# Optimization experiments

Hardware: AMD Instinct MI355X
Metric: run time of the kernel (lower is better)

The kernel has to match this reference:

```python
import jax, jax.numpy as jnp
import numpy as np

B, S, D, H = 2, 2048, 1024, 16
DK = D // H  # 64
THETA = 10000.0
SCALE = 1.0 / np.sqrt(DK)


def _rope(t, pos):
    """Apply rotary embedding. t: [b,h,s,dk], pos: [b,s] int."""
    inv_freq = THETA ** (-jnp.arange(0, DK, 2, dtype=jnp.float32) / DK)  # [dk/2]
    ang = pos[:, None, :, None].astype(jnp.float32) * inv_freq  # [b,1,s,dk/2]
    cos, sin = jnp.cos(ang), jnp.sin(ang)
    t1, t2 = t[..., 0::2], t[..., 1::2]  # interleaved pairs
    rot = jnp.stack([t1 * cos - t2 * sin, t1 * sin + t2 * cos], axis=-1)
    return rot.reshape(t.shape)


def setup_inputs() -> dict:
    key = jax.random.key(0)
    ks = jax.random.split(key, 9)
    sc = 0.02
    x = jax.random.normal(ks[0], (B, S, D), jnp.float32)
    token_position = jnp.tile(jnp.arange(S, dtype=jnp.int32)[None, :], (B, 1))
    Wq = jax.random.normal(ks[1], (D, D), jnp.float32) * sc
    Wk = jax.random.normal(ks[2], (D, D), jnp.float32) * sc
    Wv = jax.random.normal(ks[3], (D, D), jnp.float32) * sc
    Wo = jax.random.normal(ks[4], (D, D), jnp.float32) * sc
    bq = jnp.zeros((D,), jnp.float32)
    bk = jnp.zeros((D,), jnp.float32)
    bv = jnp.zeros((D,), jnp.float32)
    bo = jnp.zeros((D,), jnp.float32)
    return {"x": x, "token_position": token_position,
            "Wq": Wq, "bq": bq, "Wk": Wk, "bk": bk,
            "Wv": Wv, "bv": bv, "Wo": Wo, "bo": bo}


def reference(x, token_position, Wq, bq, Wk, bk, Wv, bv, Wo, bo):
    b, s, d = x.shape
    # projections, split heads: [b,s,d] -> [b,h,s,dk]
    def heads(t):
        return t.reshape(b, s, H, DK).transpose(0, 2, 1, 3)
    q = heads(x @ Wq + bq)
    k = heads(x @ Wk + bk)
    v = heads(x @ Wv + bv)
    q = _rope(q, token_position)
    k = _rope(k, token_position)
    scores = jnp.einsum('bhnk,bhmk->bhnm', q, k) * SCALE  # [b,h,s,s]
    causal = jnp.tril(jnp.ones((s, s), dtype=bool))
    scores = jnp.where(causal, scores, -jnp.inf)
    probs = jax.nn.softmax(scores, axis=-1)
    o = jnp.einsum('bhnm,bhmk->bhnk', probs, v)  # [b,h,s,dk]
    o = o.transpose(0, 2, 1, 3).reshape(b, s, d)
    return o @ Wo + bo
```

## Files before the change

### kernel.cpp

```cpp
#include <hip/hip_runtime.h>
#include <math.h>

#define BB  2
#define SS  2048
#define DD  1024
#define HH  16
#define DKK 64

constexpr float kScale = 0.125f;
constexpr float kC1 = 0.18033688011112042f;
constexpr float kC2 = 23.0831206542234144f;

typedef __bf16 bf16x8 __attribute__((ext_vector_type(8)));
typedef __bf16 bf16x4 __attribute__((ext_vector_type(4)));
typedef float f32x4 __attribute__((ext_vector_type(4)));

__device__ __forceinline__ void async_copy16(const void* g, void* l) {
  __builtin_amdgcn_global_load_lds(
      (const __attribute__((address_space(1))) void*)g,
      (__attribute__((address_space(3))) void*)l, 16, 0, 0);
}

__global__ __launch_bounds__(256) void prep_kernel(
    const float* __restrict__ x, const int* __restrict__ pos,
    const float* __restrict__ W0, const float* __restrict__ W1,
    const float* __restrict__ W2, const float* __restrict__ W3,
    __bf16* __restrict__ xb, float2* __restrict__ rtab,
    __bf16* __restrict__ T0, __bf16* __restrict__ T1,
    __bf16* __restrict__ T2, __bf16* __restrict__ T3) {
  __shared__ __bf16 tile[64][65];
  const int bid = blockIdx.x;
  const int t = threadIdx.x;
  if (bid < 2048) {
    const size_t i = ((size_t)bid * 256 + t) * 8;
    const float4 v0 = *(const float4*)(x + i);
    const float4 v1 = *(const float4*)(x + i + 4);
    bf16x8 o;
    o[0] = (__bf16)v0.x; o[1] = (__bf16)v0.y; o[2] = (__bf16)v0.z; o[3] = (__bf16)v0.w;
    o[4] = (__bf16)v1.x; o[5] = (__bf16)v1.y; o[6] = (__bf16)v1.z; o[7] = (__bf16)v1.w;
    *(bf16x8*)(xb + i) = o;
  } else if (bid < 2560) {
    const int idx = (bid - 2048) * 256 + t;
    const int m = idx >> 5, pi = idx & 31;
    const float inv = exp2f(-0.4152410118609203f * (float)pi);
    float sn, cs;
    __sincosf((float)pos[m] * inv, &sn, &cs);
    rtab[idx] = make_float2(cs, sn);
  } else {
    const int tid2 = bid - 2560;
    const int z = tid2 >> 8, rem = tid2 & 255;
    const float* W;
    __bf16* T;
    switch (z) {
      case 0: W = W0; T = T0; break;
      case 1: W = W1; T = T1; break;
      case 2: W = W2; T = T2; break;
      default: W = W3; T = T3; break;
    }
    const int k0 = (rem >> 4) * 64, n0 = (rem & 15) * 64;
    const int c = t & 63, rg = t >> 6;
#pragma unroll
    for (int i = 0; i < 16; i++) {
      const int r = rg + i * 4;
      tile[r][c] = (__bf16)W[(size_t)(k0 + r) * DD + n0 + c];
    }
    __syncthreads();
#pragma unroll
    for (int i = 0; i < 16; i++) {
      const int r = rg + i * 4;
      T[(size_t)(n0 + r) * DD + k0 + c] = tile[c][r];
    }
  }
}

__device__ __forceinline__ void gemm_core(
    const __bf16* __restrict__ A, const __bf16* __restrict__ Bt,
    int bm, int bn, f32x4 (&acc)[4][4], __bf16* As, __bf16* Bs) {
  const int t = threadIdx.x;
  const int lane = t & 63, wave = t >> 6;
  const int col = lane & 15, quad = lane >> 4;
  const int wm = (wave & 1) * 64, wn = (wave >> 1) * 64;

  const int r16 = lane >> 2;
  const int gch = (lane & 3) ^ ((r16 >> 1) & 3);
  const __bf16* ag = A + (size_t)(bm + wave * 32 + r16) * DD + gch * 8;
  const __bf16* bg = Bt + (size_t)(bn + wave * 32 + r16) * DD + gch * 8;
  __bf16* asb = As + wave * 1024;
  __bf16* bsb = Bs + wave * 1024;

  const int rch = (quad ^ ((col >> 1) & 3)) * 8;

  auto stage = [&](int kt, int buf) {
    const int bo = buf * 4096;
    async_copy16(ag + kt, asb + bo);
    async_copy16(ag + (size_t)16 * DD + kt, asb + bo + 512);
    async_copy16(bg + kt, bsb + bo);
    async_copy16(bg + (size_t)16 * DD + kt, bsb + bo + 512);
  };

  stage(0, 0);
  stage(32, 1);

  int rb = 0, sb = 2;
#pragma unroll 1
  for (int step = 0; step < 32; step++) {
    if (step < 31)
      asm volatile("s_waitcnt vmcnt(4)" ::: "memory");
    else
      asm volatile("s_waitcnt vmcnt(0)" ::: "memory");
    __builtin_amdgcn_s_barrier();
    asm volatile("" ::: "memory");

    const int bo = rb * 4096;
    bf16x8 af[4], bf[4];
#pragma unroll
    for (int i = 0; i < 4; i++)
      af[i] = *(const bf16x8*)(As + bo + (wm + i * 16 + col) * 32 + rch);
#pragma unroll
    for (int j = 0; j < 4; j++)
      bf[j] = *(const bf16x8*)(Bs + bo + (wn + j * 16 + col) * 32 + rch);

    if (step + 2 < 32) stage((step + 2) * 32, sb);

    __builtin_amdgcn_s_setprio(1);
#pragma unroll
    for (int i = 0; i < 4; i++)
#pragma unroll
      for (int j = 0; j < 4; j++)
        acc[i][j] =
            __builtin_amdgcn_mfma_f32_16x16x32_bf16(af[i], bf[j], acc[i][j], 0, 0, 0);
    __builtin_amdgcn_s_setprio(0);

    rb = rb == 2 ? 0 : rb + 1;
    sb = sb == 2 ? 0 : sb + 1;
  }
}

__global__ __launch_bounds__(256, 3) void qkv_gemm_kernel(
    const __bf16* __restrict__ xb, const __bf16* __restrict__ WqT,
    const __bf16* __restrict__ WkT, const __bf16* __restrict__ WvT,
    const float* __restrict__ bq, const float* __restrict__ bk,
    const float* __restrict__ bv, const float2* __restrict__ ropetab,
    __bf16* __restrict__ qo, __bf16* __restrict__ ko, __bf16* __restrict__ vo) {
  __shared__ __bf16 As[3 * 128 * 32];
  __shared__ __bf16 Bs[3 * 128 * 32];
  const int mat = blockIdx.x >> 3;
  const int bn = (blockIdx.x & 7) * 128;
  const int bm = blockIdx.y * 128;

  f32x4 acc[4][4] = {};
  const int t = threadIdx.x, lane = t & 63, wave = t >> 6;
  const int col = lane & 15, quad = lane >> 4;
  const int wm = (wave & 1) * 64, wn = (wave >> 1) * 64;

  if (mat == 2) {
    gemm_core(WvT, xb, bn, bm, acc, As, Bs);
    const int b = bm >> 11;
#pragma unroll
    for (int i = 0; i < 4; i++) {
#pragma unroll
      for (int r = 0; r < 4; r++) {
        const int n = bn + wm + i * 16 + quad * 4 + r;
        const float bb = bv[n];
        const int h = n >> 6, dk = n & 63;
        __bf16* vrow = vo + ((size_t)(b * HH + h) * DKK + dk) * SS;
#pragma unroll
        for (int j = 0; j < 4; j++) {
          const int m = bm + wn + j * 16 + col;
          vrow[m & (SS - 1)] = (__bf16)(acc[i][j][r] + bb);
        }
      }
    }
    return;
  }

  const __bf16* Bt = mat == 0 ? WqT : WkT;
  const float* bias = mat == 0 ? bq : bk;
  __bf16* out = mat == 0 ? qo : ko;
  gemm_core(xb, Bt, bm, bn, acc, As, Bs);

#pragma unroll
  for (int i = 0; i < 4; i++) {
#pragma unroll
    for (int j = 0; j < 4; j++) {
      const int n = bn + wn + j * 16 + col;
      const float bb = bias[n];
      const int pi = (n & 63) >> 1;
#pragma unroll
      for (int r = 0; r < 4; r++) {
        const int m = bm + wm + i * 16 + quad * 4 + r;
        float v = acc[i][j][r] + bb;
        {
          const float other = __shfl_xor(v, 1, 64);
          const float2 cssn = ropetab[(size_t)m * 32 + pi];
          v = (n & 1) ? (other * cssn.y + v * cssn.x)
                      : (v * cssn.x - other * cssn.y);
        }
        const int h = n >> 6, dk = n & 63;
        const int b = m >> 11, s = m & (SS - 1);
        out[((size_t)(b * HH + h) * SS + s) * DKK + dk] = (__bf16)v;
      }
    }
  }
}

__global__ __launch_bounds__(256, 3) void oproj_gemm_kernel(
    const __bf16* __restrict__ ob, const __bf16* __restrict__ WoT,
    const float* __restrict__ bo, float* __restrict__ out) {
  __shared__ __bf16 As[3 * 128 * 32];
  __shared__ __bf16 Bs[3 * 128 * 32];
  const int bn = blockIdx.x * 128;
  const int bm = blockIdx.y * 128;
  f32x4 acc[4][4] = {};
  gemm_core(ob, WoT, bm, bn, acc, As, Bs);

  const int t = threadIdx.x, lane = t & 63, wave = t >> 6;
  const int col = lane & 15, quad = lane >> 4;
  const int wm = (wave & 1) * 64, wn = (wave >> 1) * 64;
#pragma unroll
  for (int i = 0; i < 4; i++) {
#pragma unroll
    for (int j = 0; j < 4; j++) {
      const int n = bn + wn + j * 16 + col;
      const float bb = bo[n];
#pragma unroll
      for (int r = 0; r < 4; r++) {
        const int m = bm + wm + i * 16 + quad * 4 + r;
        out[(size_t)m * DD + n] = acc[i][j][r] + bb;
      }
    }
  }
}

__global__ __launch_bounds__(512, 6) void flash_attn_mfma_kernel(
    const __bf16* __restrict__ q, const __bf16* __restrict__ k,
    const __bf16* __restrict__ vt, __bf16* __restrict__ o,
    float* __restrict__ Opart, float* __restrict__ lpart) {
  __shared__ __bf16 Ks[2][64 * 64];
  __shared__ __bf16 Vs[2][64 * 64];
  __shared__ __bf16 Ps[8][16 * 72];

  const int bh = blockIdx.x;
  const int y = blockIdx.y;
  int qtile, ktBeg, ktEnd, half;
  bool isSplit;
  if (y < 14) {
    qtile = 15 - (y >> 1);
    half = y & 1;
    isSplit = true;
    ktBeg = half ? (qtile + 1) : 0;
    ktEnd = half ? (2 * qtile + 2) : (qtile + 1);
  } else {
    qtile = 22 - y;
    half = 0;
    isSplit = false;
    ktBeg = 0;
    ktEnd = 2 * qtile + 2;
  }

  const int t = threadIdx.x, lane = t & 63, wave = t >> 6;
  const int col = lane & 15, quad = lane >> 4;
  const int r8 = lane >> 3;
  const int cg = (lane & 7) ^ r8;
  const int w4 = wave & 3;

  const __bf16* qb = q + (size_t)bh * SS * DKK;
  const __bf16* kb = k + (size_t)bh * SS * DKK;
  const __bf16* vtb = vt + (size_t)bh * DKK * SS;
  const int b = bh / HH, h = bh % HH;
  __bf16* pw = (__bf16*)Ps[wave];

  const int rbase = qtile * 128 + wave * 16;
  const int myDiag = 2 * qtile + (wave >> 2);

  bf16x8 qf[2];
#pragma unroll
  for (int ks = 0; ks < 2; ks++)
    qf[ks] = *(const bf16x8*)(qb + (size_t)(rbase + col) * DKK + ks * 32 +
                              quad * 8);

  f32x4 oacc[4] = {};
  float l_lane = 0.f;

  auto stage = [&](int kt, int buf) {
    async_copy16(kb + (size_t)(kt * 64 + wave * 8 + r8) * DKK + cg * 8,
                 &Ks[buf][wave * 512]);
    async_copy16(vtb + (size_t)(wave * 8 + r8) * SS + kt * 64 + cg * 8,
                 &Vs[buf][wave * 512]);
  };

  stage(ktBeg, 0);
  __syncthreads();

  int cur = 0;
  for (int kt = ktBeg; kt < ktEnd; kt++) {
    if (kt + 1 < ktEnd) stage(kt + 1, cur ^ 1);

    if (kt <= myDiag) {
      f32x4 sc[4] = {};
      __builtin_amdgcn_s_setprio(1);
#pragma unroll
      for (int ct = 0; ct < 4; ct++)
#pragma unroll
        for (int ks = 0; ks < 2; ks++) {
          const bf16x8 kf = *(const bf16x8*)(&Ks[cur][(ct * 16 + col) * 64 +
                                             (((ks * 4 + quad) ^ (col & 7)) * 8)]);
          sc[ct] = __builtin_amdgcn_mfma_f32_16x16x32_bf16(kf, qf[ks], sc[ct],
                                                           0, 0, 0);
        }
      __builtin_amdgcn_s_setprio(0);

      if (kt < myDiag) {
#pragma unroll
        for (int ct = 0; ct < 4; ct++) {
          float p0 = exp2f(sc[ct][0] * kC1 - kC2);
          float p1 = exp2f(sc[ct][1] * kC1 - kC2);
          float p2 = exp2f(sc[ct][2] * kC1 - kC2);
          float p3 = exp2f(sc[ct][3] * kC1 - kC2);
          l_lane += (p0 + p1) + (p2 + p3);
          bf16x4 pv;
          pv[0] = (__bf16)p0; pv[1] = (__bf16)p1;
          pv[2] = (__bf16)p2; pv[3] = (__bf16)p3;
          *(bf16x4*)(pw + col * 72 + ct * 16 + quad * 4) = pv;
        }
      } else {
#pragma unroll
        for (int ct = 0; ct < 4; ct++) {
          bf16x4 pv;
          if (ct > w4) {
            pv[0] = pv[1] = pv[2] = pv[3] = (__bf16)0.0f;
          } else if (ct < w4) {
            float p0 = exp2f(sc[ct][0] * kC1 - kC2);
            float p1 = exp2f(sc[ct][1] * kC1 - kC2);
            float p2 = exp2f(sc[ct][2] * kC1 - kC2);
            float p3 = exp2f(sc[ct][3] * kC1 - kC2);
            l_lane += (p0 + p1) + (p2 + p3);
            pv[0] = (__bf16)p0; pv[1] = (__bf16)p1;
            pv[2] = (__bf16)p2; pv[3] = (__bf16)p3;
          } else {
#pragma unroll
            for (int r = 0; r < 4; r++) {
              float p = exp2f(sc[ct][r] * kC1 - kC2);
              if (quad * 4 + r > col) p = 0.0f;
              l_lane += p;
              pv[r] = (__bf16)p;
            }
          }
          *(bf16x4*)(pw + col * 72 + ct * 16 + quad * 4) = pv;
        }
      }

      {
        bf16x8 pf[2];
#pragma unroll
        for (int ks = 0; ks < 2; ks++)
          pf[ks] = *(const bf16x8*)(pw + col * 72 + ks * 32 + quad * 8);
        __builtin_amdgcn_s_setprio(1);
#pragma unroll
        for (int dt = 0; dt < 4; dt++)
#pragma unroll
          for (int ks = 0; ks < 2; ks++) {
            const bf16x8 vf = *(const bf16x8*)(&Vs[cur][(dt * 16 + col) * 64 +
                                               (((ks * 4 + quad) ^ (col & 7)) * 8)]);
            oacc[dt] = __builtin_amdgcn_mfma_f32_16x16x32_bf16(pf[ks], vf,
                                                               oacc[dt], 0, 0, 0);
          }
        __builtin_amdgcn_s_setprio(0);
      }
    }

    __syncthreads();
    cur ^= 1;
  }

  float l = l_lane;
  l += __shfl_xor(l, 16, 64);
  l += __shfl_xor(l, 32, 64);

  if (!isSplit) {
#pragma unroll
    for (int r = 0; r < 4; r++) {
      const float lr = __shfl(l, quad * 4 + r, 64);
      const float inv_l = 1.0f / lr;
      const int s = rbase + quad * 4 + r;
#pragma unroll
      for (int dt = 0; dt < 4; dt++)
        o[((size_t)(b * SS + s) * HH + h) * DKK + dt * 16 + col] =
            (__bf16)(oacc[dt][r] * inv_l);
    }
  } else {
    const int tile = (bh * 7 + (qtile - 9)) * 2 + half;
    float* Op = Opart + (size_t)tile * (128 * 64);
#pragma unroll
    for (int r = 0; r < 4; r++) {
      const int row = wave * 16 + quad * 4 + r;
#pragma unroll
      for (int dt = 0; dt < 4; dt++)
        Op[row * 64 + dt * 16 + col] = oacc[dt][r];
    }
    if (quad == 0) lpart[tile * 128 + wave * 16 + col] = l;
  }
}

__global__ __launch_bounds__(256) void combine_kernel(
    const float* __restrict__ Opart, const float* __restrict__ lpart,
    __bf16* __restrict__ o) {
  const int bh = blockIdx.x / 7, qi = blockIdx.x % 7;
  const int qtile = qi + 9;
  const int b = bh / HH, h = bh % HH;
  const int t = threadIdx.x;
  const int row = t >> 1, dk0 = (t & 1) * 32;
  const int ta = (bh * 7 + qi) * 2, tb = ta + 1;
  const float la = lpart[ta * 128 + row], lb = lpart[tb * 128 + row];
  const float inv = 1.0f / (la + lb);
  const int s = qtile * 128 + row;
  const float* Oa = Opart + (size_t)ta * 8192 + row * 64 + dk0;
  const float* Ob = Opart + (size_t)tb * 8192 + row * 64 + dk0;
  __bf16* orow = o + ((size_t)(b * SS + s) * HH + h) * DKK + dk0;
#pragma unroll
  for (int i = 0; i < 32; i += 4) {
    const float4 a = *(const float4*)(Oa + i);
    const float4 bb = *(const float4*)(Ob + i);
    orow[i + 0] = (__bf16)((a.x + bb.x) * inv);
    orow[i + 1] = (__bf16)((a.y + bb.y) * inv);
    orow[i + 2] = (__bf16)((a.z + bb.z) * inv);
    orow[i + 3] = (__bf16)((a.w + bb.w) * inv);
  }
}

extern "C" void kernel_launch(void* const* d_in, const int* in_sizes, int n_in,
                              void* d_out, int out_size, void* d_ws,
                              size_t ws_size, hipStream_t stream) {
  const float* x  = (const float*)d_in[0];
  const int*  pos = (const int*)d_in[1];
  const float* Wq = (const float*)d_in[2];
  const float* bq = (const float*)d_in[3];
  const float* Wk = (const float*)d_in[4];
  const float* bk = (const float*)d_in[5];
  const float* Wv = (const float*)d_in[6];
  const float* bv = (const float*)d_in[7];
  const float* Wo = (const float*)d_in[8];
  const float* bo = (const float*)d_in[9];
  float* out = (float*)d_out;

  char* ws = (char*)d_ws;
  __bf16* xb  = (__bf16*)(ws);
  __bf16* WqT = (__bf16*)(ws + ((size_t)8  << 20));
  __bf16* WkT = (__bf16*)(ws + ((size_t)10 << 20));
  __bf16* WvT = (__bf16*)(ws + ((size_t)12 << 20));
  __bf16* WoT = (__bf16*)(ws + ((size_t)14 << 20));
  __bf16* qb  = (__bf16*)(ws + ((size_t)16 << 20));
  __bf16* kb  = (__bf16*)(ws + ((size_t)24 << 20));
  __bf16* vtb = (__bf16*)(ws + ((size_t)32 << 20));
  __bf16* ob  = (__bf16*)(ws + ((size_t)40 << 20));
  float2* rtab = (float2*)(ws + ((size_t)48 << 20));
  float* Opart = (float*)(ws);
  float* lpart = (float*)(ws + ((size_t)48 << 20));

  prep_kernel<<<3584, 256, 0, stream>>>(x, pos, Wq, Wk, Wv, Wo, xb, rtab, WqT,
                                        WkT, WvT, WoT);
  qkv_gemm_kernel<<<dim3(24, 32), 256, 0, stream>>>(xb, WqT, WkT, WvT, bq, bk,
                                                    bv, rtab, qb, kb, vtb);
  flash_attn_mfma_kernel<<<dim3(32, 23), 512, 0, stream>>>(qb, kb, vtb, ob,
                                                           Opart, lpart);
  combine_kernel<<<224, 256, 0, stream>>>(Opart, lpart, ob);
  oproj_gemm_kernel<<<dim3(8, 32), 256, 0, stream>>>(ob, WoT, bo, out);
}
```

Baseline: 191.8 us.

## Pass attention probabilities through register shuffles instead of LDS staging

The probability tile used to be written to per-wave shared memory and read back as MFMA A-operands. Now the P values are packed to bf16 pairs and redistributed across lanes with __shfl, with QK^T and PV interleaved in two 32-key halves. This removes the Ps LDS buffer, which frees shared memory, and the launch bound is raised from 6 to 8 blocks to allow higher occupancy. The cost is extra cross-lane shuffles (ds_bpermute) and possible register pressure under the tighter launch bound.

```diff
diff --git a/kernel.cpp b/kernel.cpp
--- a/kernel.cpp
+++ b/kernel.cpp
@@ -232,13 +232,12 @@
   }
 }
 
-__global__ __launch_bounds__(512, 6) void flash_attn_mfma_kernel(
+__global__ __launch_bounds__(512, 8) void flash_attn_mfma_kernel(
     const __bf16* __restrict__ q, const __bf16* __restrict__ k,
     const __bf16* __restrict__ vt, __bf16* __restrict__ o,
     float* __restrict__ Opart, float* __restrict__ lpart) {
   __shared__ __bf16 Ks[2][64 * 64];
   __shared__ __bf16 Vs[2][64 * 64];
-  __shared__ __bf16 Ps[8][16 * 72];
 
   const int bh = blockIdx.x;
   const int y = blockIdx.y;
@@ -268,15 +267,18 @@
   const __bf16* kb = k + (size_t)bh * SS * DKK;
   const __bf16* vtb = vt + (size_t)bh * DKK * SS;
   const int b = bh / HH, h = bh % HH;
-  __bf16* pw = (__bf16*)Ps[wave];
 
   const int rbase = qtile * 128 + wave * 16;
   const int myDiag = 2 * qtile + (wave >> 2);
 
+  const int src0 = ((lane >> 4) & 1) * 32 + col;
+  const int src1 = src0 + 16;
+  const bool hi2 = quad >= 2;
+
   bf16x8 qf[2];
 #pragma unroll
-  for (int ks = 0; ks < 2; ks++)
-    qf[ks] = *(const bf16x8*)(qb + (size_t)(rbase + col) * DKK + ks * 32 +
+  for (int kk = 0; kk < 2; kk++)
+    qf[kk] = *(const bf16x8*)(qb + (size_t)(rbase + col) * DKK + kk * 32 +
                               quad * 8);
 
   f32x4 oacc[4] = {};
@@ -289,6 +291,12 @@
                  &Vs[buf][wave * 512]);
   };
 
+  union U2 { __bf16 h[2]; unsigned u; };
+  auto pk = [](float lo, float hi) {
+    U2 x; x.h[0] = (__bf16)lo; x.h[1] = (__bf16)hi; return x.u;
+  };
+  union V8 { unsigned u[4]; bf16x8 v; };
+
   stage(ktBeg, 0);
   __syncthreads();
 
@@ -297,74 +305,66 @@
     if (kt + 1 < ktEnd) stage(kt + 1, cur ^ 1);
 
     if (kt <= myDiag) {
-      f32x4 sc[4] = {};
-      __builtin_amdgcn_s_setprio(1);
-#pragma unroll
-      for (int ct = 0; ct < 4; ct++)
-#pragma unroll
-        for (int ks = 0; ks < 2; ks++) {
-          const bf16x8 kf = *(const bf16x8*)(&Ks[cur][(ct * 16 + col) * 64 +
-                                             (((ks * 4 + quad) ^ (col & 7)) * 8)]);
-          sc[ct] = __builtin_amdgcn_mfma_f32_16x16x32_bf16(kf, qf[ks], sc[ct],
-                                                           0, 0, 0);
+      const bool diag = (kt == myDiag);
+
+      auto smpack = [&](const f32x4& s, int ct, unsigned& wlo, unsigned& whi) {
+        float p0 = exp2f(s[0] * kC1 - kC2);
+        float p1 = exp2f(s[1] * kC1 - kC2);
+        float p2 = exp2f(s[2] * kC1 - kC2);
+        float p3 = exp2f(s[3] * kC1 - kC2);
+        if (diag) {
+          if (ct > w4) {
+            p0 = p1 = p2 = p3 = 0.f;
+          } else if (ct == w4) {
+            if (quad * 4 + 0 > col) p0 = 0.f;
+            if (quad * 4 + 1 > col) p1 = 0.f;
+            if (quad * 4 + 2 > col) p2 = 0.f;
+            if (quad * 4 + 3 > col) p3 = 0.f;
+          }
         }
-      __builtin_amdgcn_s_setprio(0);
-
-      if (kt < myDiag) {
-#pragma unroll
-        for (int ct = 0; ct < 4; ct++) {
-          float p0 = exp2f(sc[ct][0] * kC1 - kC2);
-          float p1 = exp2f(sc[ct][1] * kC1 - kC2);
-          float p2 = exp2f(sc[ct][2] * kC1 - kC2);
-          float p3 = exp2f(sc[ct][3] * kC1 - kC2);
-          l_lane += (p0 + p1) + (p2 + p3);
-          bf16x4 pv;
-          pv[0] = (__bf16)p0; pv[1] = (__bf16)p1;
-          pv[2] = (__bf16)p2; pv[3] = (__bf16)p3;
-          *(bf16x4*)(pw + col * 72 + ct * 16 + quad * 4) = pv;
+        l_lane += (p0 + p1) + (p2 + p3);
+        wlo = pk(p0, p1);
+        whi = pk(p2, p3);
+      };
+
+#pragma unroll
+      for (int tk = 0; tk < 2; tk++) {
+        const int ct0 = tk * 2;
+        f32x4 sa = {}, sb = {};
+        __builtin_amdgcn_s_setprio(1);
+#pragma unroll
+        for (int kk = 0; kk < 2; kk++) {
+          const bf16x8 kfa = *(const bf16x8*)(&Ks[cur][((ct0 + 0) * 16 + col) * 64 +
+                                              (((kk * 4 + quad) ^ (col & 7)) * 8)]);
+          sa = __builtin_amdgcn_mfma_f32_16x16x32_bf16(kfa, qf[kk], sa, 0, 0, 0);
+          const bf16x8 kfb = *(const bf16x8*)(&Ks[cur][((ct0 + 1) * 16 + col) * 64 +
+                                              (((kk * 4 + quad) ^ (col & 7)) * 8)]);
+          sb = __builtin_amdgcn_mfma_f32_16x16x32_bf16(kfb, qf[kk], sb, 0, 0, 0);
         }
-      } else {
-#pragma unroll
-        for (int ct = 0; ct < 4; ct++) {
-          bf16x4 pv;
-          if (ct > w4) {
-            pv[0] = pv[1] = pv[2] = pv[3] = (__bf16)0.0f;
-          } else if (ct < w4) {
-            float p0 = exp2f(sc[ct][0] * kC1 - kC2);
-            float p1 = exp2f(sc[ct][1] * kC1 - kC2);
-            float p2 = exp2f(sc[ct][2] * kC1 - kC2);
-            float p3 = exp2f(sc[ct][3] * kC1 - kC2);
-            l_lane += (p0 + p1) + (p2 + p3);
-            pv[0] = (__bf16)p0; pv[1] = (__bf16)p1;
-            pv[2] = (__bf16)p2; pv[3] = (__bf16)p3;
-          } else {
-#pragma unroll
-            for (int r = 0; r < 4; r++) {
-              float p = exp2f(sc[ct][r] * kC1 - kC2);
-              if (quad * 4 + r > col) p = 0.0f;
-              l_lane += p;
-              pv[r] = (__bf16)p;
-            }
-          }
-          *(bf16x4*)(pw + col * 72 + ct * 16 + quad * 4) = pv;
+        __builtin_amdgcn_s_setprio(0);
+
+        unsigned w00, w01, w10, w11;
+        smpack(sa, ct0 + 0, w00, w01);
+        smpack(sb, ct0 + 1, w10, w11);
+
+        const unsigned a00 = __shfl(w00, src0, 64), a01 = __shfl(w01, src0, 64);
+        const unsigned a10 = __shfl(w10, src0, 64), a11 = __shfl(w11, src0, 64);
+        const unsigned b00 = __shfl(w00, src1, 64), b01 = __shfl(w01, src1, 64);
+        const unsigned b10 = __shfl(w10, src1, 64), b11 = __shfl(w11, src1, 64);
+        V8 pf;
+        pf.u[0] = hi2 ? a10 : a00;
+        pf.u[1] = hi2 ? a11 : a01;
+        pf.u[2] = hi2 ? b10 : b00;
+        pf.u[3] = hi2 ? b11 : b01;
+
+        __builtin_amdgcn_s_setprio(1);
+#pragma unroll
+        for (int dt = 0; dt < 4; dt++) {
+          const bf16x8 vf = *(const bf16x8*)(&Vs[cur][(dt * 16 + col) * 64 +
+                                             (((tk * 4 + quad) ^ (col & 7)) * 8)]);
+          oacc[dt] = __builtin_amdgcn_mfma_f32_16x16x32_bf16(pf.v, vf,
+                                                             oacc[dt], 0, 0, 0);
         }
-      }
-
-      {
-        bf16x8 pf[2];
-#pragma unroll
-        for (int ks = 0; ks < 2; ks++)
-          pf[ks] = *(const bf16x8*)(pw + col * 72 + ks * 32 + quad * 8);
-        __builtin_amdgcn_s_setprio(1);
-#pragma unroll
-        for (int dt = 0; dt < 4; dt++)
-#pragma unroll
-          for (int ks = 0; ks < 2; ks++) {
-            const bf16x8 vf = *(const bf16x8*)(&Vs[cur][(dt * 16 + col) * 64 +
-                                               (((ks * 4 + quad) ^ (col & 7)) * 8)]);
-            oacc[dt] = __builtin_amdgcn_mfma_f32_16x16x32_bf16(pf[ks], vf,
-                                                               oacc[dt], 0, 0, 0);
-          }
         __builtin_amdgcn_s_setprio(0);
       }
     }
```

New measurement: 204.8 us. 1.07x slower.

## Fuse split-KV combine into flash attention via atomic pair counters

Applied to the files above, without the earlier changes.

Adds per-pair atomic counters, zeroed in the prep kernel, so the second finishing half of each split query tile merges its partner's partial output and normalizer itself. This removes the separate combine kernel launch and its extra pass over the partial results. In exchange it adds a thread fence, two block barriers and an atomic at the end of every split block. It only takes effect when the workspace is large enough, otherwise the old combine path still runs.

```diff
diff --git a/kernel.cpp b/kernel.cpp
--- a/kernel.cpp
+++ b/kernel.cpp
@@ -27,7 +27,8 @@
     const float* __restrict__ W2, const float* __restrict__ W3,
     __bf16* __restrict__ xb, float2* __restrict__ rtab,
     __bf16* __restrict__ T0, __bf16* __restrict__ T1,
-    __bf16* __restrict__ T2, __bf16* __restrict__ T3) {
+    __bf16* __restrict__ T2, __bf16* __restrict__ T3,
+    int* __restrict__ flags) {
   __shared__ __bf16 tile[64][65];
   const int bid = blockIdx.x;
   const int t = threadIdx.x;
@@ -40,6 +41,7 @@
     o[4] = (__bf16)v1.x; o[5] = (__bf16)v1.y; o[6] = (__bf16)v1.z; o[7] = (__bf16)v1.w;
     *(bf16x8*)(xb + i) = o;
   } else if (bid < 2560) {
+    if (flags && bid == 2048 && t < 224) flags[t] = 0;
     const int idx = (bid - 2048) * 256 + t;
     const int m = idx >> 5, pi = idx & 31;
     const float inv = exp2f(-0.4152410118609203f * (float)pi);
@@ -235,10 +237,12 @@
 __global__ __launch_bounds__(512, 6) void flash_attn_mfma_kernel(
     const __bf16* __restrict__ q, const __bf16* __restrict__ k,
     const __bf16* __restrict__ vt, __bf16* __restrict__ o,
-    float* __restrict__ Opart, float* __restrict__ lpart) {
+    float* __restrict__ Opart, float* __restrict__ lpart,
+    int* __restrict__ flags) {
   __shared__ __bf16 Ks[2][64 * 64];
   __shared__ __bf16 Vs[2][64 * 64];
   __shared__ __bf16 Ps[8][16 * 72];
+  __shared__ int who;
 
   const int bh = blockIdx.x;
   const int y = blockIdx.y;
@@ -389,7 +393,8 @@
             (__bf16)(oacc[dt][r] * inv_l);
     }
   } else {
-    const int tile = (bh * 7 + (qtile - 9)) * 2 + half;
+    const int pair = bh * 7 + (qtile - 9);
+    const int tile = pair * 2 + half;
     float* Op = Opart + (size_t)tile * (128 * 64);
 #pragma unroll
     for (int r = 0; r < 4; r++) {
@@ -399,6 +404,30 @@
         Op[row * 64 + dt * 16 + col] = oacc[dt][r];
     }
     if (quad == 0) lpart[tile * 128 + wave * 16 + col] = l;
+
+    if (flags) {
+      __threadfence();
+      __syncthreads();
+      if (t == 0) who = atomicAdd(&flags[pair], 1);
+      __syncthreads();
+      if (who == 1) {
+        __threadfence();
+        const int ptile = pair * 2 + (1 - half);
+        const float* Pp = Opart + (size_t)ptile * (128 * 64);
+        const float* lp = lpart + ptile * 128;
+#pragma unroll
+        for (int r = 0; r < 4; r++) {
+          const int row = wave * 16 + quad * 4 + r;
+          const float lr = __shfl(l, quad * 4 + r, 64) + lp[row];
+          const float inv_l = 1.0f / lr;
+          const int s = qtile * 128 + row;
+#pragma unroll
+          for (int dt = 0; dt < 4; dt++)
+            o[((size_t)(b * SS + s) * HH + h) * DKK + dt * 16 + col] =
+                (__bf16)((oacc[dt][r] + Pp[row * 64 + dt * 16 + col]) * inv_l);
+        }
+      }
+    }
   }
 }
 
@@ -456,13 +485,15 @@
   float2* rtab = (float2*)(ws + ((size_t)48 << 20));
   float* Opart = (float*)(ws);
   float* lpart = (float*)(ws + ((size_t)48 << 20));
+  const bool fused = ws_size >= (((size_t)49 << 20) + 1024);
+  int* flags = fused ? (int*)(ws + ((size_t)49 << 20)) : nullptr;
 
   prep_kernel<<<3584, 256, 0, stream>>>(x, pos, Wq, Wk, Wv, Wo, xb, rtab, WqT,
-                                        WkT, WvT, WoT);
+                                        WkT, WvT, WoT, flags);
   qkv_gemm_kernel<<<dim3(24, 32), 256, 0, stream>>>(xb, WqT, WkT, WvT, bq, bk,
                                                     bv, rtab, qb, kb, vtb);
   flash_attn_mfma_kernel<<<dim3(32, 23), 512, 0, stream>>>(qb, kb, vtb, ob,
-                                                           Opart, lpart);
-  combine_kernel<<<224, 256, 0, stream>>>(Opart, lpart, ob);
+                                                           Opart, lpart, flags);
+  if (!fused) combine_kernel<<<224, 256, 0, stream>>>(Opart, lpart, ob);
   oproj_gemm_kernel<<<dim3(8, 32), 256, 0, stream>>>(ob, WoT, bo, out);
 }
```

New measurement: 350.5 us. 82.7% more time.

## Switch flash attention to 32x32x16 MFMA with 4 waves of 32 query rows

Applied to the files above, without the earlier changes.

The attention kernel moves from eight waves each handling 16 query rows with 16x16x32 MFMAs to four waves each handling 32 rows with 32x32x16 MFMAs. The K/V staging, P buffer layout (now XOR-swizzled) and causal masking are reworked to match, and each wave skips the upper-triangle half-tile on the diagonal. The aim is fewer MFMA issues, more data reuse per wave and less LDS traffic per FLOP. In exchange, each workgroup has half the threads and more registers per lane, which lowers occupancy and latency hiding.

```diff
diff --git a/kernel.cpp b/kernel.cpp
--- a/kernel.cpp
+++ b/kernel.cpp
@@ -14,6 +14,7 @@
 typedef __bf16 bf16x8 __attribute__((ext_vector_type(8)));
 typedef __bf16 bf16x4 __attribute__((ext_vector_type(4)));
 typedef float f32x4 __attribute__((ext_vector_type(4)));
+typedef float f32x16 __attribute__((ext_vector_type(16)));
 
 __device__ __forceinline__ void async_copy16(const void* g, void* l) {
   __builtin_amdgcn_global_load_lds(
@@ -232,13 +233,13 @@
   }
 }
 
-__global__ __launch_bounds__(512, 6) void flash_attn_mfma_kernel(
+__global__ __launch_bounds__(256, 3) void flash_attn_mfma_kernel(
     const __bf16* __restrict__ q, const __bf16* __restrict__ k,
     const __bf16* __restrict__ vt, __bf16* __restrict__ o,
     float* __restrict__ Opart, float* __restrict__ lpart) {
   __shared__ __bf16 Ks[2][64 * 64];
   __shared__ __bf16 Vs[2][64 * 64];
-  __shared__ __bf16 Ps[8][16 * 72];
+  __shared__ __bf16 Ps[4][32 * 64];
 
   const int bh = blockIdx.x;
   const int y = blockIdx.y;
@@ -259,10 +260,10 @@
   }
 
   const int t = threadIdx.x, lane = t & 63, wave = t >> 6;
-  const int col = lane & 15, quad = lane >> 4;
+  const int l31 = lane & 31, hi32 = lane >> 5;
   const int r8 = lane >> 3;
   const int cg = (lane & 7) ^ r8;
-  const int w4 = wave & 3;
+  const int sw7 = l31 & 7;
 
   const __bf16* qb = q + (size_t)bh * SS * DKK;
   const __bf16* kb = k + (size_t)bh * SS * DKK;
@@ -270,23 +271,28 @@
   const int b = bh / HH, h = bh % HH;
   __bf16* pw = (__bf16*)Ps[wave];
 
-  const int rbase = qtile * 128 + wave * 16;
-  const int myDiag = 2 * qtile + (wave >> 2);
-
-  bf16x8 qf[2];
-#pragma unroll
-  for (int ks = 0; ks < 2; ks++)
-    qf[ks] = *(const bf16x8*)(qb + (size_t)(rbase + col) * DKK + ks * 32 +
-                              quad * 8);
-
-  f32x4 oacc[4] = {};
+  const int rbase = qtile * 128 + wave * 32;
+  const int myDiag = 2 * qtile + (wave >> 1);
+  const int mybase = (wave & 1) * 32;
+
+  bf16x8 qf[4];
+#pragma unroll
+  for (int kk = 0; kk < 4; kk++)
+    qf[kk] = *(const bf16x8*)(qb + (size_t)(rbase + l31) * DKK + kk * 16 +
+                              hi32 * 8);
+
+  f32x16 oa0 = {}, oa1 = {};
   float l_lane = 0.f;
 
   auto stage = [&](int kt, int buf) {
-    async_copy16(kb + (size_t)(kt * 64 + wave * 8 + r8) * DKK + cg * 8,
-                 &Ks[buf][wave * 512]);
-    async_copy16(vtb + (size_t)(wave * 8 + r8) * SS + kt * 64 + cg * 8,
-                 &Vs[buf][wave * 512]);
+#pragma unroll
+    for (int i = 0; i < 2; i++) {
+      const int slab = wave * 2 + i;
+      async_copy16(kb + (size_t)(kt * 64 + slab * 8 + r8) * DKK + cg * 8,
+                   &Ks[buf][slab * 512]);
+      async_copy16(vtb + (size_t)(slab * 8 + r8) * SS + kt * 64 + cg * 8,
+                   &Vs[buf][slab * 512]);
+    }
   };
 
   stage(ktBeg, 0);
@@ -297,108 +303,91 @@
     if (kt + 1 < ktEnd) stage(kt + 1, cur ^ 1);
 
     if (kt <= myDiag) {
-      f32x4 sc[4] = {};
-      __builtin_amdgcn_s_setprio(1);
-#pragma unroll
-      for (int ct = 0; ct < 4; ct++)
-#pragma unroll
-        for (int ks = 0; ks < 2; ks++) {
-          const bf16x8 kf = *(const bf16x8*)(&Ks[cur][(ct * 16 + col) * 64 +
-                                             (((ks * 4 + quad) ^ (col & 7)) * 8)]);
-          sc[ct] = __builtin_amdgcn_mfma_f32_16x16x32_bf16(kf, qf[ks], sc[ct],
-                                                           0, 0, 0);
-        }
-      __builtin_amdgcn_s_setprio(0);
-
-      if (kt < myDiag) {
-#pragma unroll
-        for (int ct = 0; ct < 4; ct++) {
-          float p0 = exp2f(sc[ct][0] * kC1 - kC2);
-          float p1 = exp2f(sc[ct][1] * kC1 - kC2);
-          float p2 = exp2f(sc[ct][2] * kC1 - kC2);
-          float p3 = exp2f(sc[ct][3] * kC1 - kC2);
-          l_lane += (p0 + p1) + (p2 + p3);
-          bf16x4 pv;
-          pv[0] = (__bf16)p0; pv[1] = (__bf16)p1;
-          pv[2] = (__bf16)p2; pv[3] = (__bf16)p3;
-          *(bf16x4*)(pw + col * 72 + ct * 16 + quad * 4) = pv;
-        }
-      } else {
-#pragma unroll
-        for (int ct = 0; ct < 4; ct++) {
-          bf16x4 pv;
-          if (ct > w4) {
-            pv[0] = pv[1] = pv[2] = pv[3] = (__bf16)0.0f;
-          } else if (ct < w4) {
-            float p0 = exp2f(sc[ct][0] * kC1 - kC2);
-            float p1 = exp2f(sc[ct][1] * kC1 - kC2);
-            float p2 = exp2f(sc[ct][2] * kC1 - kC2);
-            float p3 = exp2f(sc[ct][3] * kC1 - kC2);
+      const bool diag = (kt == myDiag);
+      const bool skip2nd = diag && (mybase == 0);
+
+#pragma unroll
+      for (int th = 0; th < 2; th++) {
+        if (!(skip2nd && th == 1)) {
+          f32x16 sc = {};
+          __builtin_amdgcn_s_setprio(1);
+#pragma unroll
+          for (int kk = 0; kk < 4; kk++) {
+            const bf16x8 kf = *(const bf16x8*)(
+                &Ks[cur][(th * 32 + l31) * 64 + (((kk * 2 + hi32) ^ sw7) * 8)]);
+            sc = __builtin_amdgcn_mfma_f32_32x32x16_bf16(kf, qf[kk], sc,
+                                                         0, 0, 0);
+          }
+          __builtin_amdgcn_s_setprio(0);
+
+          const bool maskh = diag && (th * 32 == mybase);
+#pragma unroll
+          for (int g = 0; g < 4; g++) {
+            float p0 = exp2f(sc[g * 4 + 0] * kC1 - kC2);
+            float p1 = exp2f(sc[g * 4 + 1] * kC1 - kC2);
+            float p2 = exp2f(sc[g * 4 + 2] * kC1 - kC2);
+            float p3 = exp2f(sc[g * 4 + 3] * kC1 - kC2);
+            if (maskh) {
+              const int tl = g * 8 + hi32 * 4;
+              if (tl + 0 > l31) p0 = 0.f;
+              if (tl + 1 > l31) p1 = 0.f;
+              if (tl + 2 > l31) p2 = 0.f;
+              if (tl + 3 > l31) p3 = 0.f;
+            }
             l_lane += (p0 + p1) + (p2 + p3);
+            bf16x4 pv;
             pv[0] = (__bf16)p0; pv[1] = (__bf16)p1;
             pv[2] = (__bf16)p2; pv[3] = (__bf16)p3;
-          } else {
-#pragma unroll
-            for (int r = 0; r < 4; r++) {
-              float p = exp2f(sc[ct][r] * kC1 - kC2);
-              if (quad * 4 + r > col) p = 0.0f;
-              l_lane += p;
-              pv[r] = (__bf16)p;
-            }
+            *(bf16x4*)(pw + l31 * 64 + (((th * 4 + g) ^ sw7) * 8) + hi32 * 4) =
+                pv;
           }
-          *(bf16x4*)(pw + col * 72 + ct * 16 + quad * 4) = pv;
         }
       }
 
-      {
-        bf16x8 pf[2];
-#pragma unroll
-        for (int ks = 0; ks < 2; ks++)
-          pf[ks] = *(const bf16x8*)(pw + col * 72 + ks * 32 + quad * 8);
-        __builtin_amdgcn_s_setprio(1);
-#pragma unroll
-        for (int dt = 0; dt < 4; dt++)
-#pragma unroll
-          for (int ks = 0; ks < 2; ks++) {
-            const bf16x8 vf = *(const bf16x8*)(&Vs[cur][(dt * 16 + col) * 64 +
-                                               (((ks * 4 + quad) ^ (col & 7)) * 8)]);
-            oacc[dt] = __builtin_amdgcn_mfma_f32_16x16x32_bf16(pf[ks], vf,
-                                                               oacc[dt], 0, 0, 0);
-          }
-        __builtin_amdgcn_s_setprio(0);
+      __builtin_amdgcn_s_setprio(1);
+#pragma unroll
+      for (int kk2 = 0; kk2 < 4; kk2++) {
+        if (!(skip2nd && kk2 >= 2)) {
+          const bf16x8 pf = *(const bf16x8*)(
+              pw + l31 * 64 + (((kk2 * 2 + hi32) ^ sw7) * 8));
+          const bf16x8 vf0 = *(const bf16x8*)(
+              &Vs[cur][l31 * 64 + (((kk2 * 2 + hi32) ^ sw7) * 8)]);
+          oa0 = __builtin_amdgcn_mfma_f32_32x32x16_bf16(pf, vf0, oa0, 0, 0, 0);
+          const bf16x8 vf1 = *(const bf16x8*)(
+              &Vs[cur][(32 + l31) * 64 + (((kk2 * 2 + hi32) ^ sw7) * 8)]);
+          oa1 = __builtin_amdgcn_mfma_f32_32x32x16_bf16(pf, vf1, oa1, 0, 0, 0);
+        }
       }
+      __builtin_amdgcn_s_setprio(0);
     }
 
     __syncthreads();
     cur ^= 1;
   }
 
-  float l = l_lane;
-  l += __shfl_xor(l, 16, 64);
-  l += __shfl_xor(l, 32, 64);
+  const float l = l_lane + __shfl_xor(l_lane, 32, 64);
 
   if (!isSplit) {
 #pragma unroll
-    for (int r = 0; r < 4; r++) {
-      const float lr = __shfl(l, quad * 4 + r, 64);
-      const float inv_l = 1.0f / lr;
-      const int s = rbase + quad * 4 + r;
-#pragma unroll
-      for (int dt = 0; dt < 4; dt++)
-        o[((size_t)(b * SS + s) * HH + h) * DKK + dt * 16 + col] =
-            (__bf16)(oacc[dt][r] * inv_l);
+    for (int reg = 0; reg < 16; reg++) {
+      const int rl = (reg & 3) + 8 * (reg >> 2) + 4 * hi32;
+      const float inv_l = 1.0f / __shfl(l, rl, 64);
+      const int s = rbase + rl;
+      __bf16* orow = o + ((size_t)(b * SS + s) * HH + h) * DKK;
+      orow[l31] = (__bf16)(oa0[reg] * inv_l);
+      orow[32 + l31] = (__bf16)(oa1[reg] * inv_l);
     }
   } else {
     const int tile = (bh * 7 + (qtile - 9)) * 2 + half;
     float* Op = Opart + (size_t)tile * (128 * 64);
 #pragma unroll
-    for (int r = 0; r < 4; r++) {
-      const int row = wave * 16 + quad * 4 + r;
-#pragma unroll
-      for (int dt = 0; dt < 4; dt++)
-        Op[row * 64 + dt * 16 + col] = oacc[dt][r];
-    }
-    if (quad == 0) lpart[tile * 128 + wave * 16 + col] = l;
+    for (int reg = 0; reg < 16; reg++) {
+      const int rl = (reg & 3) + 8 * (reg >> 2) + 4 * hi32;
+      const int row = wave * 32 + rl;
+      Op[row * 64 + l31] = oa0[reg];
+      Op[row * 64 + 32 + l31] = oa1[reg];
+    }
+    if (hi32 == 0) lpart[tile * 128 + wave * 32 + l31] = l;
   }
 }
 
@@ -461,7 +450,7 @@
                                         WkT, WvT, WoT);
   qkv_gemm_kernel<<<dim3(24, 32), 256, 0, stream>>>(xb, WqT, WkT, WvT, bq, bk,
                                                     bv, rtab, qb, kb, vtb);
-  flash_attn_mfma_kernel<<<dim3(32, 23), 512, 0, stream>>>(qb, kb, vtb, ob,
+  flash_attn_mfma_kernel<<<dim3(32, 23), 256, 0, stream>>>(qb, kb, vtb, ob,
                                                            Opart, lpart);
   combine_kernel<<<224, 256, 0, stream>>>(Opart, lpart, ob);
   oproj_gemm_kernel<<<dim3(8, 32), 256, 0, stream>>>(ob, WoT, bo, out);
```

Result: slower. 195.8 us (+2.1%).
